# Optimization experiments

Hardware: AMD Instinct MI355X
Metric: run time of the kernel (lower is better)

Reference implementation:

```python
import jax, jax.numpy as jnp
import numpy as np

D_MODEL = 2048
D_FF = 8192


def _act_quant(x):
    # BitNet b1.58 per-token int8 absmax activation quantization with STE passthrough
    scale = 127.0 / jnp.clip(jnp.max(jnp.abs(x), axis=-1, keepdims=True), 1e-5)
    xq = jnp.clip(jnp.round(x * scale), -128.0, 127.0) / scale
    return x + jax.lax.stop_gradient(xq - x)


def _weight_quant(w):
    # Ternary {-1,0,1} weight quantization with per-tensor mean-abs scale
    scale = 1.0 / jnp.clip(jnp.mean(jnp.abs(w)), 1e-5)
    wq = jnp.clip(jnp.round(w * scale), -1.0, 1.0) / scale
    return w + jax.lax.stop_gradient(wq - w)


def _bitlinear(x, w):
    # y = Q_act(x) @ Q_w(w)^T   (w has shape [out, in], torch Linear convention)
    return jnp.einsum('bsd,fd->bsf', _act_quant(x), _weight_quant(w))


def setup_inputs() -> dict:
    key = jax.random.key(0)
    k_x, k_w1, k_w2 = jax.random.split(key, 3)
    x = jax.random.normal(k_x, (4, 4096, D_MODEL), dtype=jnp.float32)
    # torch Linear default init scale ~ 1/sqrt(fan_in)
    W1 = jax.random.normal(k_w1, (D_FF, D_MODEL), dtype=jnp.float32) / np.sqrt(D_MODEL)
    W2 = jax.random.normal(k_w2, (D_MODEL, D_FF), dtype=jnp.float32) / np.sqrt(D_FF)
    return {"x": x, "W1": W1, "W2": W2}


def reference(x, W1, W2):
    h = jax.nn.silu(_bitlinear(x, W1))   # [B, S, d_ff]
    return _bitlinear(h, W2)             # [B, S, d_model]; dropout p=0 -> identity
```

## Files before the change

### kernel.cpp

```cpp
#include <hip/hip_runtime.h>
#include <hip/hip_bf16.h>
#include <cstdint>

#define DM 2048
#define DF 8192

typedef int v4i __attribute__((ext_vector_type(4)));
typedef short v8s __attribute__((ext_vector_type(8)));

__device__ __forceinline__ float silu_f(float y) {
  return y * (1.0f / (1.0f + expf(-y)));
}

__device__ __forceinline__ void gload_lds16(const void* g, void* l) {
  __builtin_amdgcn_global_load_lds(
      (const __attribute__((address_space(1))) void*)g,
      (__attribute__((address_space(3))) void*)l, 16, 0, 0);
}

__global__ __launch_bounds__(256) void abs_sum_k(const float* __restrict__ w,
                                                 float* __restrict__ partial) {
  const int t = threadIdx.x;
  const float4* wp = (const float4*)w;
  const long base = (long)blockIdx.x * 4096;
  float s = 0.f;
#pragma unroll
  for (int i = 0; i < 16; ++i) {
    float4 v = wp[base + i * 256 + t];
    s += fabsf(v.x) + fabsf(v.y) + fabsf(v.z) + fabsf(v.w);
  }
#pragma unroll
  for (int d = 1; d < 64; d <<= 1) s += __shfl_xor(s, d, 64);
  __shared__ float wsum[4];
  if ((t & 63) == 0) wsum[t >> 6] = s;
  __syncthreads();
  if (t == 0) partial[blockIdx.x] = (wsum[0] + wsum[1]) + (wsum[2] + wsum[3]);
}

__global__ __launch_bounds__(256) void finalize_scales_k(const float* __restrict__ p1,
                                                         const float* __restrict__ p2,
                                                         float* __restrict__ sc) {
  const float* p = (blockIdx.x == 0) ? p1 : p2;
  const int t = threadIdx.x;
  float s = (p[t] + p[t + 256]) + (p[t + 512] + p[t + 768]);
#pragma unroll
  for (int d = 1; d < 64; d <<= 1) s += __shfl_xor(s, d, 64);
  __shared__ float wsum[4];
  if ((t & 63) == 0) wsum[t >> 6] = s;
  __syncthreads();
  if (t == 0) {
    float total = (wsum[0] + wsum[1]) + (wsum[2] + wsum[3]);
    float mean = total * (1.0f / 16777216.0f);
    float c = fmaxf(mean, 1e-5f);
    sc[blockIdx.x * 2 + 0] = 1.0f / c;
    sc[blockIdx.x * 2 + 1] = c;
  }
}

__global__ __launch_bounds__(256) void tern_quant_k(const float* __restrict__ w,
                                                    int8_t* __restrict__ wq,
                                                    const float* __restrict__ scp) {
  const float s = scp[0];
  const long i = (long)blockIdx.x * 256 + threadIdx.x;
  float4 v = ((const float4*)w)[i];
  int q0 = (int)rintf(v.x * s); q0 = q0 < -1 ? -1 : (q0 > 1 ? 1 : q0);
  int q1 = (int)rintf(v.y * s); q1 = q1 < -1 ? -1 : (q1 > 1 ? 1 : q1);
  int q2 = (int)rintf(v.z * s); q2 = q2 < -1 ? -1 : (q2 > 1 ? 1 : q2);
  int q3 = (int)rintf(v.w * s); q3 = q3 < -1 ? -1 : (q3 > 1 ? 1 : q3);
  ((int*)wq)[i] = (q0 & 255) | ((q1 & 255) << 8) | ((q2 & 255) << 16) | ((q3 & 255) << 24);
}

__global__ __launch_bounds__(256) void act_quant_x_k(const float* __restrict__ x,
                                                     int8_t* __restrict__ xq,
                                                     float* __restrict__ inv_sx) {
  const int t = threadIdx.x;
  const long row = blockIdx.x;
  const float4* xr = (const float4*)(x + row * DM);
  float4 v0 = xr[t * 2], v1 = xr[t * 2 + 1];
  float m = fmaxf(fmaxf(fmaxf(fabsf(v0.x), fabsf(v0.y)), fmaxf(fabsf(v0.z), fabsf(v0.w))),
                  fmaxf(fmaxf(fabsf(v1.x), fabsf(v1.y)), fmaxf(fabsf(v1.z), fabsf(v1.w))));
#pragma unroll
  for (int d = 1; d < 64; d <<= 1) m = fmaxf(m, __shfl_xor(m, d, 64));
  __shared__ float wm[4];
  if ((t & 63) == 0) wm[t >> 6] = m;
  __syncthreads();
  m = fmaxf(fmaxf(wm[0], wm[1]), fmaxf(wm[2], wm[3]));
  const float scale = 127.0f / fmaxf(m, 1e-5f);
  if (t == 0) inv_sx[row] = 1.0f / scale;
  float vv[8] = {v0.x, v0.y, v0.z, v0.w, v1.x, v1.y, v1.z, v1.w};
  int q[8];
#pragma unroll
  for (int j = 0; j < 8; ++j) {
    int qq = (int)rintf(vv[j] * scale);
    q[j] = qq < -128 ? -128 : (qq > 127 ? 127 : qq);
  }
  int lo = (q[0] & 255) | ((q[1] & 255) << 8) | ((q[2] & 255) << 16) | ((q[3] & 255) << 24);
  int hi = (q[4] & 255) | ((q[5] & 255) << 8) | ((q[6] & 255) << 16) | ((q[7] & 255) << 24);
  ((int2*)(xq + row * DM))[t] = make_int2(lo, hi);
}

template <int MO, int NO>
__device__ __forceinline__ void cluster(const v4i (&af)[4][2], const v4i (&bf)[2][2],
                                        v4i (&acc)[8][4]) {
  __builtin_amdgcn_s_setprio(1);
#pragma unroll
  for (int ks = 0; ks < 2; ++ks)
#pragma unroll
    for (int m = 0; m < 4; ++m)
#pragma unroll
      for (int n = 0; n < 2; ++n)
        acc[MO + m][NO + n] = __builtin_amdgcn_mfma_i32_16x16x64_i8(
            af[m][ks], bf[n][ks], acc[MO + m][NO + n], 0, 0, 0);
  __builtin_amdgcn_s_setprio(0);
}

template <int K, int N, int EPI>
__global__ __launch_bounds__(512, 2) void gemm8_i8_k(
    const int8_t* __restrict__ A, const int8_t* __restrict__ B,
    const float* __restrict__ rowInv, const float* __restrict__ invswp,
    short* __restrict__ Y16, float* __restrict__ rowmaxP,
    float* __restrict__ Out) {
  constexpr int NT = K / 128;
  constexpr int NBX = N / 256;
  __shared__ __align__(16) uint8_t lds[131072];

  const int t = threadIdx.x;
  const int wave = t >> 6;
  const int lane = t & 63;
  const int wr = wave >> 2;
  const int wc = wave & 3;
  const int l15 = lane & 15, l4 = lane >> 4;

  const int cpx = (int)gridDim.x >> 3;
  const int bid0 = blockIdx.x;
  const int bid = (bid0 & 7) * cpx + (bid0 >> 3);
  const int bx = bid % NBX, by = bid / NBX;
  const long arow0 = (long)by * 256;
  const long bcol0 = (long)bx * 256;

  const int8_t* Ablk = A + arow0 * K;
  const int8_t* Bblk = B + bcol0 * K;

  const int srow = t >> 3;
  const int scol = ((t & 7) ^ (srow & 7)) << 4;

  const int rAo = (wr * 128 + l15) * 128;
  const int rBo = (wc * 64 + l15) * 128;
  const int sw = (l15 & 7) << 4;
  const int cc0 = (l4 * 16) ^ sw;
  const int cc1 = (64 | (l4 * 16)) ^ sw;

  v4i acc[8][4] = {};
  v4i a_lo[4][2], a_hi[4][2], b_lo[2][2], b_hi[2][2];

#define STAGE(ktile_, part_)                                                      \
  do {                                                                            \
    const int kk = (ktile_);                                                      \
    if (kk < NT) {                                                                \
      uint8_t* d0 = lds + ((kk & 1) << 16) + ((part_) << 14) + (wave << 10);      \
      const int8_t* sp = ((part_) < 2) ? Ablk : Bblk;                             \
      const int8_t* s0 =                                                          \
          sp + (long)((((part_) & 1) << 7) + srow) * K + ((long)kk << 7) + scol;  \
      gload_lds16(s0, d0);                                                        \
      gload_lds16(s0 + ((long)K << 6), d0 + 8192);                                \
    }                                                                             \
  } while (0)

#define LGKM0 asm volatile("s_waitcnt lgkmcnt(0)" ::: "memory"); \
              __builtin_amdgcn_sched_barrier(0)
#define SB    __builtin_amdgcn_sched_barrier(0)

  STAGE(0, 0); STAGE(0, 1); STAGE(0, 2); STAGE(0, 3);
  STAGE(1, 0); STAGE(1, 1);
  asm volatile("s_waitcnt vmcnt(4)" ::: "memory");
  __builtin_amdgcn_s_barrier();

  for (int kt = 0; kt < NT; ++kt) {
    const uint8_t* sA = lds + ((kt & 1) << 16);
    const uint8_t* sB = sA + 32768;

#pragma unroll
    for (int m = 0; m < 4; ++m) {
      a_lo[m][0] = *(const v4i*)(sA + rAo + m * 2048 + cc0);
      a_lo[m][1] = *(const v4i*)(sA + rAo + m * 2048 + cc1);
    }
#pragma unroll
    for (int n = 0; n < 2; ++n) {
      b_lo[n][0] = *(const v4i*)(sB + rBo + n * 2048 + cc0);
      b_lo[n][1] = *(const v4i*)(sB + rBo + n * 2048 + cc1);
    }
    STAGE(kt + 1, 2);
    LGKM0;
#pragma unroll
    for (int m = 0; m < 4; ++m) {
      a_hi[m][0] = *(const v4i*)(sA + rAo + (m + 4) * 2048 + cc0);
      a_hi[m][1] = *(const v4i*)(sA + rAo + (m + 4) * 2048 + cc1);
    }
    STAGE(kt + 1, 3);
    SB;
    cluster<0, 0>(a_lo, b_lo, acc);
    LGKM0;
#pragma unroll
    for (int n = 0; n < 2; ++n) {
      b_hi[n][0] = *(const v4i*)(sB + rBo + (n + 2) * 2048 + cc0);
      b_hi[n][1] = *(const v4i*)(sB + rBo + (n + 2) * 2048 + cc1);
    }
    __builtin_amdgcn_s_barrier();
    STAGE(kt + 2, 0);
    SB;
    cluster<4, 0>(a_hi, b_lo, acc);
    LGKM0;
    STAGE(kt + 2, 1);
    SB;
    cluster<0, 2>(a_lo, b_hi, acc);
    cluster<4, 2>(a_hi, b_hi, acc);
    if (kt < NT - 2) {
      asm volatile("s_waitcnt vmcnt(4)" ::: "memory");
    } else if (kt == NT - 2) {
      asm volatile("s_waitcnt vmcnt(0)" ::: "memory");
    }
    __builtin_amdgcn_s_barrier();
  }

  const float invsw = invswp[0];
  if constexpr (EPI == 1) {
    __syncthreads();
#pragma unroll
    for (int mi = 0; mi < 8; ++mi) {
#pragma unroll
      for (int r = 0; r < 4; ++r) {
        const int row = wr * 128 + mi * 16 + l4 * 4 + r;
#pragma unroll
        for (int ni = 0; ni < 4; ++ni) {
          int yi = acc[mi][ni][r];
          int ys = yi < -32767 ? -32767 : (yi > 32767 ? 32767 : yi);
          const int col = wc * 64 + ni * 16 + l15;
          const int byte = (row * 512 + col * 2) ^ ((row & 7) << 4);
          *(short*)(lds + byte) = (short)ys;
        }
      }
    }
    __syncthreads();
    const int row = t >> 1;
    const int half = t & 1;
    const long grow = arow0 + row;
    const float c1v = rowInv[grow] * invsw;
    float mx = 0.f;
    short* gp = Y16 + grow * (long)DF + bcol0 + half * 128;
#pragma unroll
    for (int i = 0; i < 16; ++i) {
      const int byte = (row * 512 + half * 256 + i * 16) ^ ((row & 7) << 4);
      v8s yv = *(const v8s*)(lds + byte);
#pragma unroll
      for (int j = 0; j < 8; ++j) {
        float h = silu_f((float)yv[j] * c1v);
        mx = fmaxf(mx, fabsf(h));
      }
      *(v8s*)(gp + i * 8) = yv;
    }
    mx = fmaxf(mx, __shfl_xor(mx, 1, 64));
    if (half == 0) rowmaxP[grow * NBX + bx] = mx;
  } else {
#pragma unroll
    for (int mi = 0; mi < 8; ++mi) {
#pragma unroll
      for (int r = 0; r < 4; ++r) {
        const long grow = arow0 + wr * 128 + mi * 16 + l4 * 4 + r;
        const float c2 = rowInv[grow] * invsw;
#pragma unroll
        for (int ni = 0; ni < 4; ++ni)
          Out[grow * N + bcol0 + wc * 64 + ni * 16 + l15] = (float)acc[mi][ni][r] * c2;
      }
    }
  }
#undef STAGE
#undef LGKM0
#undef SB
}

__global__ __launch_bounds__(256) void quant_h_k(const short* __restrict__ Y16,
                                                 const float* __restrict__ rowmaxP,
                                                 const float* __restrict__ inv_sx,
                                                 const float* __restrict__ sc,
                                                 int8_t* __restrict__ hq,
                                                 float* __restrict__ inv_sh) {
  const int t = threadIdx.x;
  const long row = blockIdx.x;
  __shared__ float smax_s;
  if (t < 64) {
    float m = (t < 32) ? rowmaxP[row * 32 + t] : 0.f;
#pragma unroll
    for (int d = 1; d < 64; d <<= 1) m = fmaxf(m, __shfl_xor(m, d, 64));
    if (t == 0) smax_s = m;
  }
  __syncthreads();
  const float scale = 127.0f / fmaxf(smax_s, 1e-5f);
  if (t == 0) inv_sh[row] = 1.0f / scale;
  const float c1 = inv_sx[row] * sc[1];
  const short4* yp = (const short4*)(Y16 + row * DF);
  int* op = (int*)(hq + row * DF);
#pragma unroll
  for (int b = 0; b < 8; ++b) {
    short4 s4 = yp[b * 256 + t];
    short vals[4] = {s4.x, s4.y, s4.z, s4.w};
    int q[4];
#pragma unroll
    for (int j = 0; j < 4; ++j) {
      float h = silu_f((float)vals[j] * c1);
      int qq = (int)rintf(h * scale);
      q[j] = qq < -128 ? -128 : (qq > 127 ? 127 : qq);
    }
    op[b * 256 + t] = (q[0] & 255) | ((q[1] & 255) << 8) | ((q[2] & 255) << 16) | ((q[3] & 255) << 24);
  }
}

extern "C" void kernel_launch(void* const* d_in, const int* in_sizes, int n_in,
                              void* d_out, int out_size, void* d_ws, size_t ws_size,
                              hipStream_t stream) {
  const float* x = (const float*)d_in[0];
  const float* W1 = (const float*)d_in[1];
  const float* W2 = (const float*)d_in[2];
  float* out = (float*)d_out;

  uint8_t* w = (uint8_t*)d_ws;
  float* sc = (float*)(w + 0);
  float* p1 = (float*)(w + 256);
  float* p2 = (float*)(w + 256 + 4096);
  float* inv_sx = (float*)(w + 8448);
  float* inv_sh = (float*)(w + 8448 + 65536);
  float* rowmaxP = (float*)(w + 8448 + 131072);
  uint8_t* w1q = w + 8448 + 131072 + 4194304;
  uint8_t* w2q = w1q + 16777216;
  uint8_t* xq = w2q + 16777216;
  uint8_t* hq = xq + 33554432;
  short* y16 = (short*)(hq + 134217728);

  abs_sum_k<<<1024, 256, 0, stream>>>(W1, p1);
  abs_sum_k<<<1024, 256, 0, stream>>>(W2, p2);
  finalize_scales_k<<<2, 256, 0, stream>>>(p1, p2, sc);
  tern_quant_k<<<16384, 256, 0, stream>>>(W1, (int8_t*)w1q, sc + 0);
  tern_quant_k<<<16384, 256, 0, stream>>>(W2, (int8_t*)w2q, sc + 2);
  act_quant_x_k<<<16384, 256, 0, stream>>>(x, (int8_t*)xq, inv_sx);
  gemm8_i8_k<2048, 8192, 1><<<2048, 512, 0, stream>>>(
      (const int8_t*)xq, (const int8_t*)w1q, inv_sx, sc + 1, y16, rowmaxP, nullptr);
  quant_h_k<<<16384, 256, 0, stream>>>(y16, rowmaxP, inv_sx, sc, (int8_t*)hq, inv_sh);
  gemm8_i8_k<8192, 2048, 0><<<512, 512, 0, stream>>>(
      (const int8_t*)hq, (const int8_t*)w2q, inv_sh, sc + 3, nullptr, nullptr, out);
}
```

Before: 803.3 us.

## Move SiLU row-max from GEMM1 epilogue into quant kernel; supertile block mapping

The per-row SiLU absmax is no longer computed in the first GEMM's epilogue, so that epilogue only stores the int16 results. The quant kernel now computes SiLU once into registers, reduces the row max across the block, and quantizes from the same registers. This removes a second SiLU pass and the rowmaxP partial buffer, at the cost of holding 32 floats per thread. The GEMM also remaps block ids into 8x4 supertiles to improve L2 reuse of the A and B tiles.

```diff
diff --git a/kernel.cpp b/kernel.cpp
--- a/kernel.cpp
+++ b/kernel.cpp
@@ -118,10 +118,10 @@
 __global__ __launch_bounds__(512, 2) void gemm8_i8_k(
     const int8_t* __restrict__ A, const int8_t* __restrict__ B,
     const float* __restrict__ rowInv, const float* __restrict__ invswp,
-    short* __restrict__ Y16, float* __restrict__ rowmaxP,
-    float* __restrict__ Out) {
+    short* __restrict__ Y16, float* __restrict__ Out) {
   constexpr int NT = K / 128;
   constexpr int NBX = N / 256;
+  constexpr int NSTX = NBX / 4;
   __shared__ __align__(16) uint8_t lds[131072];
 
   const int t = threadIdx.x;
@@ -134,7 +134,9 @@
   const int cpx = (int)gridDim.x >> 3;
   const int bid0 = blockIdx.x;
   const int bid = (bid0 & 7) * cpx + (bid0 >> 3);
-  const int bx = bid % NBX, by = bid / NBX;
+  const int st = bid >> 5, u = bid & 31;
+  const int by = (st / NSTX) * 8 + (u >> 2);
+  const int bx = (st % NSTX) * 4 + (u & 3);
   const long arow0 = (long)by * 256;
   const long bcol0 = (long)bx * 256;
 
@@ -222,7 +224,6 @@
     __builtin_amdgcn_s_barrier();
   }
 
-  const float invsw = invswp[0];
   if constexpr (EPI == 1) {
     __syncthreads();
 #pragma unroll
@@ -235,32 +236,21 @@
           int yi = acc[mi][ni][r];
           int ys = yi < -32767 ? -32767 : (yi > 32767 ? 32767 : yi);
           const int col = wc * 64 + ni * 16 + l15;
-          const int byte = (row * 512 + col * 2) ^ ((row & 7) << 4);
-          *(short*)(lds + byte) = (short)ys;
+          *(short*)(lds + ((row * 512 + col * 2) ^ ((row & 7) << 4))) = (short)ys;
         }
       }
     }
     __syncthreads();
     const int row = t >> 1;
     const int half = t & 1;
-    const long grow = arow0 + row;
-    const float c1v = rowInv[grow] * invsw;
-    float mx = 0.f;
-    short* gp = Y16 + grow * (long)DF + bcol0 + half * 128;
+    short* gp = Y16 + (arow0 + row) * (long)DF + bcol0 + half * 128;
 #pragma unroll
     for (int i = 0; i < 16; ++i) {
-      const int byte = (row * 512 + half * 256 + i * 16) ^ ((row & 7) << 4);
-      v8s yv = *(const v8s*)(lds + byte);
-#pragma unroll
-      for (int j = 0; j < 8; ++j) {
-        float h = silu_f((float)yv[j] * c1v);
-        mx = fmaxf(mx, fabsf(h));
-      }
+      v8s yv = *(const v8s*)(lds + ((row * 512 + half * 256 + i * 16) ^ ((row & 7) << 4)));
       *(v8s*)(gp + i * 8) = yv;
     }
-    mx = fmaxf(mx, __shfl_xor(mx, 1, 64));
-    if (half == 0) rowmaxP[grow * NBX + bx] = mx;
   } else {
+    const float invsw = invswp[0];
 #pragma unroll
     for (int mi = 0; mi < 8; ++mi) {
 #pragma unroll
@@ -279,38 +269,46 @@
 }
 
 __global__ __launch_bounds__(256) void quant_h_k(const short* __restrict__ Y16,
-                                                 const float* __restrict__ rowmaxP,
                                                  const float* __restrict__ inv_sx,
                                                  const float* __restrict__ sc,
                                                  int8_t* __restrict__ hq,
                                                  float* __restrict__ inv_sh) {
   const int t = threadIdx.x;
   const long row = blockIdx.x;
-  __shared__ float smax_s;
-  if (t < 64) {
-    float m = (t < 32) ? rowmaxP[row * 32 + t] : 0.f;
-#pragma unroll
-    for (int d = 1; d < 64; d <<= 1) m = fmaxf(m, __shfl_xor(m, d, 64));
-    if (t == 0) smax_s = m;
-  }
+  const float c1 = inv_sx[row] * sc[1];
+  const v8s* yp = (const v8s*)(Y16 + row * DF);
+  float h[32];
+  float mx = 0.f;
+#pragma unroll
+  for (int b = 0; b < 4; ++b) {
+    v8s s8 = yp[b * 256 + t];
+#pragma unroll
+    for (int j = 0; j < 8; ++j) {
+      float hv = silu_f((float)s8[j] * c1);
+      h[b * 8 + j] = hv;
+      mx = fmaxf(mx, fabsf(hv));
+    }
+  }
+#pragma unroll
+  for (int d = 1; d < 64; d <<= 1) mx = fmaxf(mx, __shfl_xor(mx, d, 64));
+  __shared__ float wm[4];
+  if ((t & 63) == 0) wm[t >> 6] = mx;
   __syncthreads();
-  const float scale = 127.0f / fmaxf(smax_s, 1e-5f);
+  const float m = fmaxf(fmaxf(wm[0], wm[1]), fmaxf(wm[2], wm[3]));
+  const float scale = 127.0f / fmaxf(m, 1e-5f);
   if (t == 0) inv_sh[row] = 1.0f / scale;
-  const float c1 = inv_sx[row] * sc[1];
-  const short4* yp = (const short4*)(Y16 + row * DF);
-  int* op = (int*)(hq + row * DF);
-#pragma unroll
-  for (int b = 0; b < 8; ++b) {
-    short4 s4 = yp[b * 256 + t];
-    short vals[4] = {s4.x, s4.y, s4.z, s4.w};
-    int q[4];
-#pragma unroll
-    for (int j = 0; j < 4; ++j) {
-      float h = silu_f((float)vals[j] * c1);
-      int qq = (int)rintf(h * scale);
+  int2* op = (int2*)(hq + row * DF);
+#pragma unroll
+  for (int b = 0; b < 4; ++b) {
+    int q[8];
+#pragma unroll
+    for (int j = 0; j < 8; ++j) {
+      int qq = (int)rintf(h[b * 8 + j] * scale);
       q[j] = qq < -128 ? -128 : (qq > 127 ? 127 : qq);
     }
-    op[b * 256 + t] = (q[0] & 255) | ((q[1] & 255) << 8) | ((q[2] & 255) << 16) | ((q[3] & 255) << 24);
+    int lo = (q[0] & 255) | ((q[1] & 255) << 8) | ((q[2] & 255) << 16) | ((q[3] & 255) << 24);
+    int hi = (q[4] & 255) | ((q[5] & 255) << 8) | ((q[6] & 255) << 16) | ((q[7] & 255) << 24);
+    op[b * 256 + t] = make_int2(lo, hi);
   }
 }
 
@@ -328,7 +326,6 @@
   float* p2 = (float*)(w + 256 + 4096);
   float* inv_sx = (float*)(w + 8448);
   float* inv_sh = (float*)(w + 8448 + 65536);
-  float* rowmaxP = (float*)(w + 8448 + 131072);
   uint8_t* w1q = w + 8448 + 131072 + 4194304;
   uint8_t* w2q = w1q + 16777216;
   uint8_t* xq = w2q + 16777216;
@@ -342,8 +339,8 @@
   tern_quant_k<<<16384, 256, 0, stream>>>(W2, (int8_t*)w2q, sc + 2);
   act_quant_x_k<<<16384, 256, 0, stream>>>(x, (int8_t*)xq, inv_sx);
   gemm8_i8_k<2048, 8192, 1><<<2048, 512, 0, stream>>>(
-      (const int8_t*)xq, (const int8_t*)w1q, inv_sx, sc + 1, y16, rowmaxP, nullptr);
-  quant_h_k<<<16384, 256, 0, stream>>>(y16, rowmaxP, inv_sx, sc, (int8_t*)hq, inv_sh);
+      (const int8_t*)xq, (const int8_t*)w1q, nullptr, nullptr, y16, nullptr);
+  quant_h_k<<<16384, 256, 0, stream>>>(y16, inv_sx, sc, (int8_t*)hq, inv_sh);
   gemm8_i8_k<8192, 2048, 0><<<512, 512, 0, stream>>>(
-      (const int8_t*)hq, (const int8_t*)w2q, inv_sh, sc + 3, nullptr, nullptr, out);
-}
+      (const int8_t*)hq, (const int8_t*)w2q, inv_sh, sc + 3, nullptr, out);
+}
```

Measured after the change: 885.4 us. 10.2% more time.
